# Optimization experiments

Measured on AMD Instinct MI355X. Metric: run time of the kernel, lower is better.

Reference implementation:

```python
import jax, jax.numpy as jnp
import numpy as np

HID = 512
NUM_NODES = 100000
N_BATCH = 20000


def _gru_cell(x, h, W_ih, W_hh, b_ih, b_hh):
    # torch nn.GRU single-step cell; gate order r, z, n
    gi = x @ W_ih.T + b_ih            # [N, 3H]
    gh = h @ W_hh.T + b_hh            # [N, 3H]
    i_r, i_z, i_n = jnp.split(gi, 3, axis=-1)
    h_r, h_z, h_n = jnp.split(gh, 3, axis=-1)
    r = jax.nn.sigmoid(i_r + h_r)
    z = jax.nn.sigmoid(i_z + h_z)
    n = jnp.tanh(i_n + r * h_n)
    return (1.0 - z) * n + z * h


def setup_inputs() -> dict:
    key = jax.random.key(0)
    ks = jax.random.split(key, 12)
    s = 1.0 / np.sqrt(HID)
    inp = {
        'conv_emb': jax.random.normal(ks[0], (N_BATCH, HID), jnp.float32),
        'static_table': jax.random.normal(ks[1], (NUM_NODES, HID), jnp.float32),
        'dynamic_table': jax.random.normal(ks[2], (NUM_NODES, 2, HID), jnp.float32),
        'W_ih0': jax.random.normal(ks[3], (3 * HID, 2 * HID), jnp.float32) * s,
        'W_hh0': jax.random.normal(ks[4], (3 * HID, HID), jnp.float32) * s,
        'b_ih0': jax.random.normal(ks[5], (3 * HID,), jnp.float32) * s,
        'b_hh0': jax.random.normal(ks[6], (3 * HID,), jnp.float32) * s,
        'W_ih1': jax.random.normal(ks[7], (3 * HID, HID), jnp.float32) * s,
        'W_hh1': jax.random.normal(ks[8], (3 * HID, HID), jnp.float32) * s,
        'b_ih1': jax.random.normal(ks[9], (3 * HID,), jnp.float32) * s,
        'b_hh1': jax.random.normal(ks[10], (3 * HID,), jnp.float32) * s,
        'nids': jnp.arange(N_BATCH, dtype=jnp.int32),  # unique global node ids
    }
    return inp


def reference(conv_emb, static_table, dynamic_table,
              W_ih0, W_hh0, b_ih0, b_hh0,
              W_ih1, W_hh1, b_ih1, b_hh1, nids):
    # gather: static embeddings for batch nodes, concat with conv output
    x = jnp.concatenate([conv_emb, static_table[nids]], axis=-1)  # [N, 2H]
    h0 = dynamic_table[nids]                                      # [N, L, H]
    # single-step 2-layer GRU (seq_len == 1)
    h_new0 = _gru_cell(x, h0[:, 0], W_ih0, W_hh0, b_ih0, b_hh0)   # [N, H]
    h_new1 = _gru_cell(h_new0, h0[:, 1], W_ih1, W_hh1, b_ih1, b_hh1)
    hn = jnp.stack([h_new0, h_new1], axis=1)                      # [N, L, H]
    # scatter updated hidden states back into the persistent table
    updated_table = dynamic_table.at[nids].set(hn)                # [num_nodes, L, H]
    return updated_table
```

## Files before the change

### kernel.cpp

```cpp
#include <hip/hip_runtime.h>

#define NB 20000
#define NNODES 100000
#define MB2 79
#define MP2 (MB2*256)
#define NBITW 3125
#define NGEMM (MB2*8)

typedef unsigned short u16;
typedef __bf16 bf16x8 __attribute__((ext_vector_type(8)));
typedef float f32x4 __attribute__((ext_vector_type(4)));

__device__ __forceinline__ u16 f2bf(float f) {
  union { float f; unsigned u; } v; v.f = f;
  unsigned r = v.u + 0x7fffu + ((v.u >> 16) & 1u);
  return (u16)(r >> 16);
}
__device__ __forceinline__ float bf2f(u16 b) {
  union { unsigned u; float f; } v; v.u = ((unsigned)b) << 16;
  return v.f;
}

template <int N> __device__ __forceinline__ void vmwaitc() {
  if constexpr (N == 0) asm volatile("s_waitcnt vmcnt(0)" ::: "memory");
  else if constexpr (N == 4) asm volatile("s_waitcnt vmcnt(4)" ::: "memory");
  else asm volatile("s_waitcnt vmcnt(8)" ::: "memory");
  __builtin_amdgcn_sched_barrier(0);
}
__device__ __forceinline__ void bar() {
  __builtin_amdgcn_sched_barrier(0);
  __builtin_amdgcn_s_barrier();
  __builtin_amdgcn_sched_barrier(0);
}

__global__ void prep_bt0i(const float* __restrict__ Wih, const float* __restrict__ Whh,
                          u16* __restrict__ Bt) {
  int idx = blockIdx.x * 256 + threadIdx.x;
  if (idx >= 2048 * 384) return;
  int jg = idx / 384;
  int k = (idx % 384) * 4;
  int j = jg >> 2, g = jg & 3;
  float4 v = make_float4(0.f, 0.f, 0.f, 0.f);
  if (g < 2) {
    int row = g * 512 + j;
    v = (k < 1024) ? *(const float4*)(Wih + (size_t)row * 1024 + k)
                   : *(const float4*)(Whh + (size_t)row * 512 + (k - 1024));
  } else if (g == 2) {
    if (k < 1024) v = *(const float4*)(Wih + (size_t)(1024 + j) * 1024 + k);
  } else {
    if (k >= 1024) v = *(const float4*)(Whh + (size_t)(1024 + j) * 512 + (k - 1024));
  }
  ushort4 b; b.x = f2bf(v.x); b.y = f2bf(v.y); b.z = f2bf(v.z); b.w = f2bf(v.w);
  *(ushort4*)(Bt + (size_t)jg * 1536 + k) = b;
}

__global__ void prep_bt1i(const float* __restrict__ Wih, const float* __restrict__ Whh,
                          u16* __restrict__ Bt) {
  int idx = blockIdx.x * 256 + threadIdx.x;
  if (idx >= 2048 * 256) return;
  int jg = idx / 256;
  int k = (idx % 256) * 4;
  int j = jg >> 2, g = jg & 3;
  float4 v = make_float4(0.f, 0.f, 0.f, 0.f);
  if (g < 2) {
    int row = g * 512 + j;
    v = (k < 512) ? *(const float4*)(Wih + (size_t)row * 512 + k)
                  : *(const float4*)(Whh + (size_t)row * 512 + (k - 512));
  } else if (g == 2) {
    if (k < 512) v = *(const float4*)(Wih + (size_t)(1024 + j) * 512 + k);
  } else {
    if (k >= 512) v = *(const float4*)(Whh + (size_t)(1024 + j) * 512 + (k - 512));
  }
  ushort4 b; b.x = f2bf(v.x); b.y = f2bf(v.y); b.z = f2bf(v.z); b.w = f2bf(v.w);
  *(ushort4*)(Bt + (size_t)jg * 1024 + k) = b;
}

__global__ void prep_a(const float* __restrict__ conv, const float* __restrict__ stat,
                       const float* __restrict__ dyn, const int* __restrict__ nids,
                       u16* __restrict__ A0, u16* __restrict__ A1) {
  int idx = blockIdx.x * 256 + threadIdx.x;
  int n = idx >> 9;
  int c = (idx & 511) * 4;
  if (n >= MP2) return;
  float4 v = make_float4(0.f, 0.f, 0.f, 0.f);
  if (n < NB) {
    size_t nid = (size_t)nids[n];
    if (c < 512)        v = *(const float4*)(conv + (size_t)n * 512 + c);
    else if (c < 1024)  v = *(const float4*)(stat + nid * 512 + (c - 512));
    else if (c < 1536)  v = *(const float4*)(dyn + nid * 1024 + (c - 1024));
    else                v = *(const float4*)(dyn + nid * 1024 + 512 + (c - 1536));
  }
  ushort4 b; b.x = f2bf(v.x); b.y = f2bf(v.y); b.z = f2bf(v.z); b.w = f2bf(v.w);
  if (c < 1536) *(ushort4*)(A0 + (size_t)n * 1536 + c) = b;
  else          *(ushort4*)(A1 + (size_t)n * 1024 + (c - 1024)) = b;
  if (n >= NB && c < 512) *(ushort4*)(A1 + (size_t)n * 1024 + c) = b;
}

__global__ void zero_bits(unsigned* __restrict__ bits) {
  int i = blockIdx.x * 256 + threadIdx.x;
  if (i < NBITW) bits[i] = 0;
}
__global__ void set_bits(const int* __restrict__ nids, unsigned* __restrict__ bits) {
  int i = blockIdx.x * 256 + threadIdx.x;
  if (i < NB) {
    int nid = nids[i];
    atomicOr(&bits[nid >> 5], 1u << (nid & 31));
  }
}

template <int K, int LAYER>
__global__ __launch_bounds__(512, 2)
void gemm4(const u16* __restrict__ A, const u16* __restrict__ Bt,
           const float* __restrict__ bih, const float* __restrict__ bhh,
           const u16* __restrict__ hsrc, int hstride, const int* __restrict__ nids,
           u16* __restrict__ a1out, float* __restrict__ out) {
  constexpr int NT = K / 32;
  __shared__ u16 S[4][16384];

  int bid = blockIdx.x;
  int bn = bid & 7, bm = bid >> 3;

  int t = threadIdx.x;
  int lane = t & 63, w = t >> 6;
  int fr = lane & 15, fq = lane >> 4;
  int wm = w >> 2, wn = w & 3;

  const u16* Ap = A + (size_t)bm * 256 * K;
  const u16* Bp = Bt + (size_t)bn * 256 * K;

  int goff[4]; int gsel[4];
  {
#pragma unroll
    for (int l = 0; l < 4; ++l) {
      int c = l * 512 + t;
      gsel[l] = c >> 10;
      int cm = c & 1023;
      int pair = cm >> 3, s = cm & 7;
      int u = s ^ (pair & 7);
      int row = pair * 2 + (u & 1);
      goff[l] = row * K + (u >> 1) * 8;
    }
  }
  auto stage = [&](int kt) {
    char* base = (char*)S + (size_t)(kt & 3) * 32768;
#pragma unroll
    for (int l = 0; l < 4; ++l) {
      const u16* g = (gsel[l] ? Bp : Ap) + goff[l] + kt * 32;
      __builtin_amdgcn_global_load_lds((const __attribute__((address_space(1))) void*)g,
                                       (__attribute__((address_space(3))) void*)
                                       (base + (l * 512 + t) * 16), 16, 0, 0);
    }
  };

  int offA[8], offB[4];
#pragma unroll
  for (int mi = 0; mi < 8; ++mi)
    offA[mi] = (wm * 64 + mi * 8 + (fr >> 1)) * 128 +
               (((fq * 2 + (fr & 1)) ^ (fr >> 1)) << 4);
#pragma unroll
  for (int nf = 0; nf < 4; ++nf)
    offB[nf] = 16384 + (wn * 32 + nf * 8 + (fr >> 1)) * 128 +
               (((fq * 2 + (fr & 1)) ^ (fr >> 1)) << 4);

  f32x4 acc[8][4] = {};

  stage(0); stage(1); stage(2);
  vmwaitc<8>();
  bar();

  for (int kt = 0; kt < NT; ++kt) {
    const char* sb = (const char*)S + (size_t)(kt & 3) * 32768;
    bf16x8 bv[4], af[8];
#pragma unroll
    for (int nf = 0; nf < 4; ++nf) bv[nf] = *(const bf16x8*)(sb + offB[nf]);
#pragma unroll
    for (int mi = 0; mi < 8; ++mi) af[mi] = *(const bf16x8*)(sb + offA[mi]);

    if (kt + 3 < NT) stage(kt + 3);

    bar();
    __builtin_amdgcn_s_setprio(1);
#pragma unroll
    for (int mi = 0; mi < 8; ++mi)
#pragma unroll
      for (int nf = 0; nf < 4; ++nf)
        acc[mi][nf] = __builtin_amdgcn_mfma_f32_16x16x32_bf16(af[mi], bv[nf],
                                                              acc[mi][nf], 0, 0, 0);
    __builtin_amdgcn_s_setprio(0);

    if (kt < NT - 3)       vmwaitc<8>();
    else if (kt == NT - 3) vmwaitc<4>();
    else if (kt == NT - 2) vmwaitc<0>();
    bar();
  }

  int gg = fr & 3, jj = fr >> 2;
  float bias[4];
#pragma unroll
  for (int nf = 0; nf < 4; ++nf) {
    int j = bn * 64 + wn * 16 + nf * 4 + jj;
    bias[nf] = (gg == 0) ? bih[j] + bhh[j]
             : (gg == 1) ? bih[512 + j] + bhh[512 + j]
             : (gg == 2) ? bih[1024 + j] : bhh[1024 + j];
  }
#pragma unroll
  for (int mi = 0; mi < 8; ++mi) {
    int row = bm * 256 + wm * 128 + mi * 16 + fq * 4 + gg;
#pragma unroll
    for (int nf = 0; nf < 4; ++nf) {
      float v[4], v1[4], v2[4];
#pragma unroll
      for (int r = 0; r < 4; ++r) v[r] = acc[mi][nf][r] + bias[nf];
#pragma unroll
      for (int i = 0; i < 4; ++i) {
        float o = __shfl_xor(v[i ^ 2], 2);
        v1[i] = ((i ^ gg) & 2) ? o : v[i];
      }
#pragma unroll
      for (int i = 0; i < 4; ++i) {
        float o = __shfl_xor(v1[i ^ 1], 1);
        v2[i] = ((i ^ gg) & 1) ? o : v1[i];
      }
      if (row < NB) {
        int j = bn * 64 + wn * 16 + nf * 4 + jj;
        float rr = 1.f / (1.f + __expf(-v2[0]));
        float zz = 1.f / (1.f + __expf(-v2[1]));
        float nn = tanhf(fmaf(rr, v2[3], v2[2]));
        float h = bf2f(hsrc[(size_t)row * hstride + j]);
        float hp = (1.f - zz) * nn + zz * h;
        if (LAYER == 0) a1out[(size_t)row * 1024 + j] = f2bf(hp);
        out[(size_t)nids[row] * 1024 + LAYER * 512 + j] = hp;
      }
    }
  }
}

__global__ void copy_skip(const float4* __restrict__ src, float4* __restrict__ dst,
                          const unsigned* __restrict__ bits) {
  const size_t total = (size_t)NNODES * 256;
  for (size_t i = (size_t)blockIdx.x * 256 + threadIdx.x; i < total;
       i += (size_t)gridDim.x * 256) {
    int row = (int)(i >> 8);
    if (!((bits[row >> 5] >> (row & 31)) & 1u)) dst[i] = src[i];
  }
}

extern "C" void kernel_launch(void* const* d_in, const int* in_sizes, int n_in,
                              void* d_out, int out_size, void* d_ws, size_t ws_size,
                              hipStream_t stream) {
  const float* conv = (const float*)d_in[0];
  const float* stat = (const float*)d_in[1];
  const float* dyn  = (const float*)d_in[2];
  const float* Wih0 = (const float*)d_in[3];
  const float* Whh0 = (const float*)d_in[4];
  const float* bih0 = (const float*)d_in[5];
  const float* bhh0 = (const float*)d_in[6];
  const float* Wih1 = (const float*)d_in[7];
  const float* Whh1 = (const float*)d_in[8];
  const float* bih1 = (const float*)d_in[9];
  const float* bhh1 = (const float*)d_in[10];
  const int*   nids = (const int*)d_in[11];
  float* out = (float*)d_out;

  char* ws = (char*)d_ws;
  u16* A0  = (u16*)ws;
  u16* A1  = (u16*)(ws + 62128128);
  u16* Bt0 = (u16*)(ws + 103546880);
  u16* Bt1 = (u16*)(ws + 109838336);
  unsigned* bits = (unsigned*)(ws + 114032640);

  zero_bits<<<(NBITW + 255) / 256, 256, 0, stream>>>(bits);
  set_bits<<<(NB + 255) / 256, 256, 0, stream>>>(nids, bits);
  prep_bt0i<<<3072, 256, 0, stream>>>(Wih0, Whh0, Bt0);
  prep_bt1i<<<2048, 256, 0, stream>>>(Wih1, Whh1, Bt1);
  prep_a<<<(MP2 * 512) / 256, 256, 0, stream>>>(conv, stat, dyn, nids, A0, A1);

  gemm4<1536, 0><<<NGEMM, 512, 0, stream>>>(A0, Bt0, bih0, bhh0,
                                            A0 + 1024, 1536, nids, A1, out);
  gemm4<1024, 1><<<NGEMM, 512, 0, stream>>>(A1, Bt1, bih1, bhh1,
                                            A1 + 512, 1024, nids, (u16*)nullptr, out);

  copy_skip<<<2048, 256, 0, stream>>>((const float4*)dyn, (float4*)out, bits);
}
```

Before: 537.7 us.

## Replace 256x256 pipelined GEMM with 128x128 single-buffered tiles and grouped block order

Both GRU GEMMs now use 128x128 output tiles computed by 256-thread blocks instead of 256x256 tiles on 512-thread blocks. The 4-stage LDS ring, manual vmcnt waits and priority hints are replaced by a single 16KB buffer with two __syncthreads per k-step. Block indices are remapped so that consecutive blocks sweep the M dimension for a fixed N tile. The aim is higher occupancy (three blocks per CU) and better L2 locality on the weight tiles. The cost is less data reuse per tile and no overlap between global loads and MFMA work.

```diff
diff --git a/kernel.cpp b/kernel.cpp
--- a/kernel.cpp
+++ b/kernel.cpp
@@ -5,7 +5,9 @@
 #define MB2 79
 #define MP2 (MB2*256)
 #define NBITW 3125
-#define NGEMM (MB2*8)
+#define MBG 157
+#define NBN 16
+#define NGEMM (MBG*NBN)
 
 typedef unsigned short u16;
 typedef __bf16 bf16x8 __attribute__((ext_vector_type(8)));
@@ -19,18 +21,6 @@
 __device__ __forceinline__ float bf2f(u16 b) {
   union { unsigned u; float f; } v; v.u = ((unsigned)b) << 16;
   return v.f;
-}
-
-template <int N> __device__ __forceinline__ void vmwaitc() {
-  if constexpr (N == 0) asm volatile("s_waitcnt vmcnt(0)" ::: "memory");
-  else if constexpr (N == 4) asm volatile("s_waitcnt vmcnt(4)" ::: "memory");
-  else asm volatile("s_waitcnt vmcnt(8)" ::: "memory");
-  __builtin_amdgcn_sched_barrier(0);
-}
-__device__ __forceinline__ void bar() {
-  __builtin_amdgcn_sched_barrier(0);
-  __builtin_amdgcn_s_barrier();
-  __builtin_amdgcn_sched_barrier(0);
 }
 
 __global__ void prep_bt0i(const float* __restrict__ Wih, const float* __restrict__ Whh,
@@ -109,103 +99,86 @@
 }
 
 template <int K, int LAYER>
-__global__ __launch_bounds__(512, 2)
-void gemm4(const u16* __restrict__ A, const u16* __restrict__ Bt,
+__global__ __launch_bounds__(256, 3)
+void gemmh(const u16* __restrict__ A, const u16* __restrict__ Bt,
            const float* __restrict__ bih, const float* __restrict__ bhh,
            const u16* __restrict__ hsrc, int hstride, const int* __restrict__ nids,
            u16* __restrict__ a1out, float* __restrict__ out) {
   constexpr int NT = K / 32;
-  __shared__ u16 S[4][16384];
+  __shared__ u16 S[8192];
 
   int bid = blockIdx.x;
-  int bn = bid & 7, bm = bid >> 3;
+  int gidx = (bid & 7) * (NGEMM / 8) + (bid >> 3);
+  int bn = gidx / MBG;
+  int bm = gidx - bn * MBG;
 
   int t = threadIdx.x;
   int lane = t & 63, w = t >> 6;
   int fr = lane & 15, fq = lane >> 4;
-  int wm = w >> 2, wn = w & 3;
-
-  const u16* Ap = A + (size_t)bm * 256 * K;
-  const u16* Bp = Bt + (size_t)bn * 256 * K;
-
-  int goff[4]; int gsel[4];
-  {
-#pragma unroll
-    for (int l = 0; l < 4; ++l) {
-      int c = l * 512 + t;
-      gsel[l] = c >> 10;
-      int cm = c & 1023;
-      int pair = cm >> 3, s = cm & 7;
-      int u = s ^ (pair & 7);
-      int row = pair * 2 + (u & 1);
-      goff[l] = row * K + (u >> 1) * 8;
-    }
-  }
-  auto stage = [&](int kt) {
-    char* base = (char*)S + (size_t)(kt & 3) * 32768;
+  int wr = w >> 1, wc = w & 1;
+
+  const u16* Ap = A + (size_t)bm * 128 * K;
+  const u16* Bp = Bt + (size_t)bn * 128 * K;
+
+  int goff[4], gsel[4];
+#pragma unroll
+  for (int l = 0; l < 4; ++l) {
+    int c = l * 256 + t;
+    gsel[l] = c >> 9;
+    int cm = c & 511;
+    int pair = cm >> 3, s = cm & 7;
+    int u = s ^ (pair & 7);
+    goff[l] = (pair * 2 + (u & 1)) * K + (u >> 1) * 8;
+  }
+
+  int offA[4], offB[4];
+#pragma unroll
+  for (int mi = 0; mi < 4; ++mi)
+    offA[mi] = (wr * 32 + mi * 8 + (fr >> 1)) * 128 +
+               (((fq * 2 + (fr & 1)) ^ ((fr >> 1) & 7)) << 4);
+#pragma unroll
+  for (int nf = 0; nf < 4; ++nf)
+    offB[nf] = 8192 + (wc * 32 + nf * 8 + (fr >> 1)) * 128 +
+               (((fq * 2 + (fr & 1)) ^ ((fr >> 1) & 7)) << 4);
+
+  f32x4 acc[4][4] = {};
+
+  for (int kt = 0; kt < NT; ++kt) {
 #pragma unroll
     for (int l = 0; l < 4; ++l) {
       const u16* g = (gsel[l] ? Bp : Ap) + goff[l] + kt * 32;
       __builtin_amdgcn_global_load_lds((const __attribute__((address_space(1))) void*)g,
                                        (__attribute__((address_space(3))) void*)
-                                       (base + (l * 512 + t) * 16), 16, 0, 0);
+                                       ((char*)S + (l * 256 + t) * 16), 16, 0, 0);
     }
-  };
-
-  int offA[8], offB[4];
-#pragma unroll
-  for (int mi = 0; mi < 8; ++mi)
-    offA[mi] = (wm * 64 + mi * 8 + (fr >> 1)) * 128 +
-               (((fq * 2 + (fr & 1)) ^ (fr >> 1)) << 4);
-#pragma unroll
-  for (int nf = 0; nf < 4; ++nf)
-    offB[nf] = 16384 + (wn * 32 + nf * 8 + (fr >> 1)) * 128 +
-               (((fq * 2 + (fr & 1)) ^ (fr >> 1)) << 4);
-
-  f32x4 acc[8][4] = {};
-
-  stage(0); stage(1); stage(2);
-  vmwaitc<8>();
-  bar();
-
-  for (int kt = 0; kt < NT; ++kt) {
-    const char* sb = (const char*)S + (size_t)(kt & 3) * 32768;
-    bf16x8 bv[4], af[8];
-#pragma unroll
-    for (int nf = 0; nf < 4; ++nf) bv[nf] = *(const bf16x8*)(sb + offB[nf]);
-#pragma unroll
-    for (int mi = 0; mi < 8; ++mi) af[mi] = *(const bf16x8*)(sb + offA[mi]);
-
-    if (kt + 3 < NT) stage(kt + 3);
-
-    bar();
-    __builtin_amdgcn_s_setprio(1);
-#pragma unroll
-    for (int mi = 0; mi < 8; ++mi)
+    __syncthreads();
+
+    bf16x8 af[4], bv[4];
+#pragma unroll
+    for (int mi = 0; mi < 4; ++mi) af[mi] = *(const bf16x8*)((const char*)S + offA[mi]);
+#pragma unroll
+    for (int nf = 0; nf < 4; ++nf) bv[nf] = *(const bf16x8*)((const char*)S + offB[nf]);
+#pragma unroll
+    for (int mi = 0; mi < 4; ++mi)
 #pragma unroll
       for (int nf = 0; nf < 4; ++nf)
         acc[mi][nf] = __builtin_amdgcn_mfma_f32_16x16x32_bf16(af[mi], bv[nf],
                                                               acc[mi][nf], 0, 0, 0);
-    __builtin_amdgcn_s_setprio(0);
-
-    if (kt < NT - 3)       vmwaitc<8>();
-    else if (kt == NT - 3) vmwaitc<4>();
-    else if (kt == NT - 2) vmwaitc<0>();
-    bar();
+    __syncthreads();
   }
 
   int gg = fr & 3, jj = fr >> 2;
   float bias[4];
 #pragma unroll
   for (int nf = 0; nf < 4; ++nf) {
-    int j = bn * 64 + wn * 16 + nf * 4 + jj;
+    int j = bn * 32 + wc * 16 + nf * 4 + jj;
     bias[nf] = (gg == 0) ? bih[j] + bhh[j]
              : (gg == 1) ? bih[512 + j] + bhh[512 + j]
              : (gg == 2) ? bih[1024 + j] : bhh[1024 + j];
   }
 #pragma unroll
-  for (int mi = 0; mi < 8; ++mi) {
-    int row = bm * 256 + wm * 128 + mi * 16 + fq * 4 + gg;
+  for (int mi = 0; mi < 4; ++mi) {
+    int row = bm * 128 + wr * 64 + mi * 16 + fq * 4 + gg;
 #pragma unroll
     for (int nf = 0; nf < 4; ++nf) {
       float v[4], v1[4], v2[4];
@@ -222,7 +195,7 @@
         v2[i] = ((i ^ gg) & 1) ? o : v1[i];
       }
       if (row < NB) {
-        int j = bn * 64 + wn * 16 + nf * 4 + jj;
+        int j = bn * 32 + wc * 16 + nf * 4 + jj;
         float rr = 1.f / (1.f + __expf(-v2[0]));
         float zz = 1.f / (1.f + __expf(-v2[1]));
         float nn = tanhf(fmaf(rr, v2[3], v2[2]));
@@ -241,7 +214,9 @@
   for (size_t i = (size_t)blockIdx.x * 256 + threadIdx.x; i < total;
        i += (size_t)gridDim.x * 256) {
     int row = (int)(i >> 8);
-    if (!((bits[row >> 5] >> (row & 31)) & 1u)) dst[i] = src[i];
+    if (!((bits[row >> 5] >> (row & 31)) & 1u)) {
+      dst[i] = src[i];
+    }
   }
 }
 
@@ -275,9 +250,9 @@
   prep_bt1i<<<2048, 256, 0, stream>>>(Wih1, Whh1, Bt1);
   prep_a<<<(MP2 * 512) / 256, 256, 0, stream>>>(conv, stat, dyn, nids, A0, A1);
 
-  gemm4<1536, 0><<<NGEMM, 512, 0, stream>>>(A0, Bt0, bih0, bhh0,
+  gemmh<1536, 0><<<NGEMM, 256, 0, stream>>>(A0, Bt0, bih0, bhh0,
                                             A0 + 1024, 1536, nids, A1, out);
-  gemm4<1024, 1><<<NGEMM, 512, 0, stream>>>(A1, Bt1, bih1, bhh1,
+  gemmh<1024, 1><<<NGEMM, 256, 0, stream>>>(A1, Bt1, bih1, bhh1,
                                             A1 + 512, 1024, nids, (u16*)nullptr, out);
 
   copy_skip<<<2048, 256, 0, stream>>>((const float4*)dyn, (float4*)out, bits);
```

After: 547.9 us. About the same (+1.9%).

## Vectorize GRU epilogue stores, change LDS swizzle, drop mid-loop barrier

Applied to the files above, without the earlier changes.

The fused GEMM+GRU epilogue now computes the gates first, then uses extra cross-lane shuffles to transpose the z and n values. Each lane can then load four h values with a single ushort4 read and write four outputs as one float4 (plus one ushort4 for layer 0). Before, every element was a separate scalar load and store. The LDS swizzle pattern changes to a new XOR scheme that is applied consistently on the write and read sides. One barrier between the LDS fragment reads and the MFMAs is removed, which relies on the end-of-iteration barrier to protect buffer reuse. The extra shuffles cost some ALU work, and the barrier removal makes the synchronisation margin tighter.

```diff
diff --git a/kernel.cpp b/kernel.cpp
--- a/kernel.cpp
+++ b/kernel.cpp
@@ -110,7 +110,7 @@
 
 template <int K, int LAYER>
 __global__ __launch_bounds__(512, 2)
-void gemm4(const u16* __restrict__ A, const u16* __restrict__ Bt,
+void gemmr(const u16* __restrict__ A, const u16* __restrict__ Bt,
            const float* __restrict__ bih, const float* __restrict__ bhh,
            const u16* __restrict__ hsrc, int hstride, const int* __restrict__ nids,
            u16* __restrict__ a1out, float* __restrict__ out) {
@@ -128,39 +128,36 @@
   const u16* Ap = A + (size_t)bm * 256 * K;
   const u16* Bp = Bt + (size_t)bn * 256 * K;
 
-  int goff[4]; int gsel[4];
-  {
-#pragma unroll
-    for (int l = 0; l < 4; ++l) {
-      int c = l * 512 + t;
-      gsel[l] = c >> 10;
-      int cm = c & 1023;
-      int pair = cm >> 3, s = cm & 7;
-      int u = s ^ (pair & 7);
-      int row = pair * 2 + (u & 1);
-      goff[l] = row * K + (u >> 1) * 8;
-    }
+  int goff[4], gsel[4];
+#pragma unroll
+  for (int l = 0; l < 4; ++l) {
+    int c = l * 512 + t;
+    gsel[l] = c >> 10;
+    int cm = c & 1023;
+    int p = cm >> 3, up = cm & 7;
+    int u = up ^ ((p & 3) << 1);
+    goff[l] = (2 * p + (u & 1)) * K + (u >> 1) * 8;
   }
   auto stage = [&](int kt) {
     char* base = (char*)S + (size_t)(kt & 3) * 32768;
 #pragma unroll
     for (int l = 0; l < 4; ++l) {
       const u16* g = (gsel[l] ? Bp : Ap) + goff[l] + kt * 32;
-      __builtin_amdgcn_global_load_lds((const __attribute__((address_space(1))) void*)g,
-                                       (__attribute__((address_space(3))) void*)
-                                       (base + (l * 512 + t) * 16), 16, 0, 0);
+      __builtin_amdgcn_global_load_lds(
+          (const __attribute__((address_space(1))) void*)g,
+          (__attribute__((address_space(3))) void*)
+          (base + (l * 512 + t) * 16), 16, 0, 0);
     }
   };
 
+  int uu = ((fq << 1) | (fr & 1)) ^ (((fr >> 1) & 3) << 1);
   int offA[8], offB[4];
 #pragma unroll
   for (int mi = 0; mi < 8; ++mi)
-    offA[mi] = (wm * 64 + mi * 8 + (fr >> 1)) * 128 +
-               (((fq * 2 + (fr & 1)) ^ (fr >> 1)) << 4);
+    offA[mi] = (wm * 64 + mi * 8 + (fr >> 1)) * 128 + uu * 16;
 #pragma unroll
   for (int nf = 0; nf < 4; ++nf)
-    offB[nf] = 16384 + (wn * 32 + nf * 8 + (fr >> 1)) * 128 +
-               (((fq * 2 + (fr & 1)) ^ (fr >> 1)) << 4);
+    offB[nf] = 16384 + ((wn >> 1) * 64 + (wn & 1) * 32 + nf * 8 + (fr >> 1)) * 128 + uu * 16;
 
   f32x4 acc[8][4] = {};
 
@@ -170,15 +167,15 @@
 
   for (int kt = 0; kt < NT; ++kt) {
     const char* sb = (const char*)S + (size_t)(kt & 3) * 32768;
-    bf16x8 bv[4], af[8];
+
+    bf16x8 af[8], bv[4];
+#pragma unroll
+    for (int mi = 0; mi < 8; ++mi) af[mi] = *(const bf16x8*)(sb + offA[mi]);
 #pragma unroll
     for (int nf = 0; nf < 4; ++nf) bv[nf] = *(const bf16x8*)(sb + offB[nf]);
-#pragma unroll
-    for (int mi = 0; mi < 8; ++mi) af[mi] = *(const bf16x8*)(sb + offA[mi]);
 
     if (kt + 3 < NT) stage(kt + 3);
 
-    bar();
     __builtin_amdgcn_s_setprio(1);
 #pragma unroll
     for (int mi = 0; mi < 8; ++mi)
@@ -188,17 +185,18 @@
                                                               acc[mi][nf], 0, 0, 0);
     __builtin_amdgcn_s_setprio(0);
 
-    if (kt < NT - 3)       vmwaitc<8>();
-    else if (kt == NT - 3) vmwaitc<4>();
-    else if (kt == NT - 2) vmwaitc<0>();
+    if (kt + 3 < NT)       vmwaitc<8>();
+    else if (kt + 3 == NT) vmwaitc<4>();
+    else if (kt + 2 == NT) vmwaitc<0>();
     bar();
   }
 
   int gg = fr & 3, jj = fr >> 2;
+  const int jbase = bn * 64 + wn * 16;
   float bias[4];
 #pragma unroll
   for (int nf = 0; nf < 4; ++nf) {
-    int j = bn * 64 + wn * 16 + nf * 4 + jj;
+    int j = jbase + nf * 4 + jj;
     bias[nf] = (gg == 0) ? bih[j] + bhh[j]
              : (gg == 1) ? bih[512 + j] + bhh[512 + j]
              : (gg == 2) ? bih[1024 + j] : bhh[1024 + j];
@@ -206,6 +204,7 @@
 #pragma unroll
   for (int mi = 0; mi < 8; ++mi) {
     int row = bm * 256 + wm * 128 + mi * 16 + fq * 4 + gg;
+    float zv[4], nv[4];
 #pragma unroll
     for (int nf = 0; nf < 4; ++nf) {
       float v[4], v1[4], v2[4];
@@ -221,15 +220,37 @@
         float o = __shfl_xor(v1[i ^ 1], 1);
         v2[i] = ((i ^ gg) & 1) ? o : v1[i];
       }
-      if (row < NB) {
-        int j = bn * 64 + wn * 16 + nf * 4 + jj;
-        float rr = 1.f / (1.f + __expf(-v2[0]));
-        float zz = 1.f / (1.f + __expf(-v2[1]));
-        float nn = tanhf(fmaf(rr, v2[3], v2[2]));
-        float h = bf2f(hsrc[(size_t)row * hstride + j]);
-        float hp = (1.f - zz) * nn + zz * h;
-        if (LAYER == 0) a1out[(size_t)row * 1024 + j] = f2bf(hp);
-        out[(size_t)nids[row] * 1024 + LAYER * 512 + j] = hp;
+      float rr = 1.f / (1.f + __expf(-v2[0]));
+      zv[nf] = 1.f / (1.f + __expf(-v2[1]));
+      nv[nf] = tanhf(fmaf(rr, v2[3], v2[2]));
+    }
+    float z1[4], z2[4], n1[4], n2[4];
+#pragma unroll
+    for (int i = 0; i < 4; ++i) {
+      float oz = __shfl_xor(zv[i ^ 2], 8);
+      float on = __shfl_xor(nv[i ^ 2], 8);
+      z1[i] = ((i ^ jj) & 2) ? oz : zv[i];
+      n1[i] = ((i ^ jj) & 2) ? on : nv[i];
+    }
+#pragma unroll
+    for (int i = 0; i < 4; ++i) {
+      float oz = __shfl_xor(z1[i ^ 1], 4);
+      float on = __shfl_xor(n1[i ^ 1], 4);
+      z2[i] = ((i ^ jj) & 1) ? oz : z1[i];
+      n2[i] = ((i ^ jj) & 1) ? on : n1[i];
+    }
+    if (row < NB) {
+      int j4 = jbase + jj * 4;
+      ushort4 hv = *(const ushort4*)(hsrc + (size_t)row * hstride + j4);
+      float hp0 = fmaf(z2[0], bf2f(hv.x) - n2[0], n2[0]);
+      float hp1 = fmaf(z2[1], bf2f(hv.y) - n2[1], n2[1]);
+      float hp2 = fmaf(z2[2], bf2f(hv.z) - n2[2], n2[2]);
+      float hp3 = fmaf(z2[3], bf2f(hv.w) - n2[3], n2[3]);
+      size_t nid = (size_t)nids[row];
+      *(float4*)(out + nid * 1024 + LAYER * 512 + j4) = make_float4(hp0, hp1, hp2, hp3);
+      if (LAYER == 0) {
+        ushort4 ob; ob.x = f2bf(hp0); ob.y = f2bf(hp1); ob.z = f2bf(hp2); ob.w = f2bf(hp3);
+        *(ushort4*)(a1out + (size_t)row * 1024 + j4) = ob;
       }
     }
   }
@@ -241,7 +262,9 @@
   for (size_t i = (size_t)blockIdx.x * 256 + threadIdx.x; i < total;
        i += (size_t)gridDim.x * 256) {
     int row = (int)(i >> 8);
-    if (!((bits[row >> 5] >> (row & 31)) & 1u)) dst[i] = src[i];
+    if (!((bits[row >> 5] >> (row & 31)) & 1u)) {
+      dst[i] = src[i];
+    }
   }
 }
 
@@ -275,9 +298,9 @@
   prep_bt1i<<<2048, 256, 0, stream>>>(Wih1, Whh1, Bt1);
   prep_a<<<(MP2 * 512) / 256, 256, 0, stream>>>(conv, stat, dyn, nids, A0, A1);
 
-  gemm4<1536, 0><<<NGEMM, 512, 0, stream>>>(A0, Bt0, bih0, bhh0,
+  gemmr<1536, 0><<<NGEMM, 512, 0, stream>>>(A0, Bt0, bih0, bhh0,
                                             A0 + 1024, 1536, nids, A1, out);
-  gemm4<1024, 1><<<NGEMM, 512, 0, stream>>>(A1, Bt1, bih1, bhh1,
+  gemmr<1024, 1><<<NGEMM, 512, 0, stream>>>(A1, Bt1, bih1, bhh1,
                                             A1 + 512, 1024, nids, (u16*)nullptr, out);
 
   copy_skip<<<2048, 256, 0, stream>>>((const float4*)dyn, (float4*)out, bits);
```

After: 501.9 us. -6.7%, faster.
